# Kernel tuning notes

Measured on AMD Instinct MI355X. Metric: run time of the kernel, lower is better.

The kernel has to match this reference:

```python
import jax, jax.numpy as jnp
import numpy as np
from jax import lax

K, N = 256, 65536

def setup_inputs() -> dict:
    key = jax.random.key(0)
    k1, k2, k3 = jax.random.split(key, 3)
    # obs: non-negative event counts [K, N]
    obs = jax.random.uniform(k1, (K, N), dtype=jnp.float32) * 4.0
    # Beta ~ U(1, 3) [K]
    Beta = 1.0 + 2.0 * jax.random.uniform(k2, (K,), dtype=jnp.float32)
    # Alpha ~ U(0, 0.01) [K, K]
    Alpha = 0.01 * jax.random.uniform(k3, (K, K), dtype=jnp.float32)
    return {"obs": obs, "Beta": Beta, "Alpha": Alpha}

def reference(obs, Beta, Alpha):
    # obs: [K, N], Beta: [K], Alpha: [K, K]
    Kk, Nn = obs.shape
    Mu0 = obs.mean(axis=1) / 10.0 + 0.01            # [K] background rate
    decay = jnp.exp(-Beta)                          # [K]

    # Exponential kernel sum S[t] = sum_{tp<t} obs[:,tp] * Beta * exp(-(t-tp)*Beta)
    # admits recursion H[t] = exp(-Beta) * (H[t-1] + obs[:, t-1]), S[t] = Beta * H[t]
    def step(h, o_prev):
        h_new = decay * (h + o_prev)
        return h_new, h_new

    _, H = lax.scan(step, jnp.zeros((Kk,), obs.dtype), obs[:, :Nn - 1].T)  # [N-1, K]
    S = H * Beta                                    # [N-1, K]
    # lam1[:, t] = softplus(Alpha @ S[t]) for t >= 1; lam1[:, 0] = 0 (by original code)
    lam = jax.nn.softplus(jnp.einsum('jk,tk->tj', Alpha, S))  # [N-1, K]
    lams1 = jnp.concatenate([jnp.zeros((Kk, 1), obs.dtype), lam.T], axis=1)  # [K, N]
    lams0 = jnp.broadcast_to(Mu0[:, None], (Kk, Nn))          # [K, N]

    Nloglams = obs * jnp.log(lams0 + lams1 + 1e-5)
    loglik = (Nloglams - lams0 - lams1).sum()
    return loglik, lams0, lams1
```

## Files before the change

kernel.cpp:

```cpp
#include <hip/hip_runtime.h>
#include <math.h>

#define KK 256
#define NN 65536
#define TT 64
#define WW 48
#define TPAD 264

typedef __bf16 bf16x8 __attribute__((ext_vector_type(8)));
typedef float f32x4 __attribute__((ext_vector_type(4)));

__global__ __launch_bounds__(256) void rowsum_kernel(const float* __restrict__ obs,
                                                     float* __restrict__ partial) {
  const int b = blockIdx.x;
  const int r = b >> 3, e = b & 7;
  const int tid = threadIdx.x;
  const float4* p = (const float4*)(obs + (size_t)r * NN + e * 8192) + tid;
  float s = 0.f;
#pragma unroll
  for (int i = 0; i < 8; ++i) {
    float4 v = p[i * 256];
    s += (v.x + v.y) + (v.z + v.w);
  }
  __shared__ float red[256];
  red[tid] = s;
  __syncthreads();
  for (int off = 128; off > 0; off >>= 1) {
    if (tid < off) red[tid] += red[tid + off];
    __syncthreads();
  }
  if (tid == 0) partial[b] = red[0];
}

__global__ __launch_bounds__(256) void prep_kernel(const float* __restrict__ Alpha,
                                                   const float* __restrict__ partial,
                                                   float* __restrict__ mu0,
                                                   __bf16* __restrict__ AlphaB,
                                                   float* __restrict__ out) {
  const int j = blockIdx.x;
  const int tid = threadIdx.x;
  AlphaB[(size_t)j * KK + tid] = (__bf16)Alpha[(size_t)j * KK + tid];
  if (tid == 0) {
    float s = 0.f;
#pragma unroll
    for (int i = 0; i < 8; ++i) s += partial[j * 8 + i];
    mu0[j] = s * (1.0f / NN) * 0.1f + 0.01f;
    if (j == 0) out[0] = 0.f;
  }
}

__global__ __launch_bounds__(256, 2) void main_kernel(const float* __restrict__ obs,
                                                      const float* __restrict__ Beta,
                                                      const float* __restrict__ mu0,
                                                      const __bf16* __restrict__ AlphaB,
                                                      float* __restrict__ out) {
  __shared__ __bf16 Slds[TT][TPAD];
  const int tid = threadIdx.x;
  const int t0 = blockIdx.x * TT;

  {
    const int k = tid;
    const float beta = Beta[k];
    const float decay = expf(-beta);
    const float* row = obs + (size_t)k * NN;
    float g = 0.f;
    if (t0 > 0) {
      const float4* p = (const float4*)(row + t0 - WW);
#pragma unroll
      for (int i = 0; i < WW / 4; ++i) {
        float4 v = p[i];
        g = decay * (g + v.x);
        g = decay * (g + v.y);
        g = decay * (g + v.z);
        g = decay * (g + v.w);
      }
    }
    Slds[0][k] = (__bf16)(beta * g);
    const float4* q = (const float4*)(row + t0);
#pragma unroll
    for (int i = 0; i < 15; ++i) {
      float4 v = q[i];
      g = decay * (g + v.x); Slds[4 * i + 1][k] = (__bf16)(beta * g);
      g = decay * (g + v.y); Slds[4 * i + 2][k] = (__bf16)(beta * g);
      g = decay * (g + v.z); Slds[4 * i + 3][k] = (__bf16)(beta * g);
      g = decay * (g + v.w); Slds[4 * i + 4][k] = (__bf16)(beta * g);
    }
    {
      float4 v = q[15];
      g = decay * (g + v.x); Slds[61][k] = (__bf16)(beta * g);
      g = decay * (g + v.y); Slds[62][k] = (__bf16)(beta * g);
      g = decay * (g + v.z); Slds[63][k] = (__bf16)(beta * g);
    }
  }
  __syncthreads();

  const int wave = tid >> 6;
  const int lane = tid & 63;
  const int lquad = lane >> 4;
  const int l16 = lane & 15;

  f32x4 acc[4][4];
#pragma unroll
  for (int a = 0; a < 4; ++a)
#pragma unroll
    for (int b = 0; b < 4; ++b) acc[a][b] = (f32x4){0.f, 0.f, 0.f, 0.f};

  const __bf16* Abase = AlphaB + (size_t)(wave * 64 + l16) * KK + lquad * 8;
  for (int k0 = 0; k0 < KK; k0 += 32) {
    bf16x8 afrag[4], bfrag[4];
#pragma unroll
    for (int js = 0; js < 4; ++js)
      afrag[js] = *(const bf16x8*)(Abase + (size_t)js * 16 * KK + k0);
#pragma unroll
    for (int ts = 0; ts < 4; ++ts)
      bfrag[ts] = *(const bf16x8*)&Slds[ts * 16 + l16][k0 + lquad * 8];
#pragma unroll
    for (int js = 0; js < 4; ++js)
#pragma unroll
      for (int ts = 0; ts < 4; ++ts)
        acc[js][ts] = __builtin_amdgcn_mfma_f32_16x16x32_bf16(
            afrag[js], bfrag[ts], acc[js][ts], 0, 0, 0);
  }

  float partial = 0.f;
  float* lams0 = out + 1;
  float* lams1 = out + 1 + (size_t)KK * NN;
#pragma unroll
  for (int js = 0; js < 4; ++js) {
#pragma unroll
    for (int r = 0; r < 4; ++r) {
      const int j = wave * 64 + js * 16 + lquad * 4 + r;
      const float m = mu0[j];
      const size_t rowoff = (size_t)j * NN + t0 + l16;
#pragma unroll
      for (int ts = 0; ts < 4; ++ts) {
        float v = acc[js][ts][r];
        float lam = v + __logf(1.f + __expf(-v));
        if (t0 + ts * 16 + l16 == 0) lam = 0.f;
        lams1[rowoff + ts * 16] = lam;
        lams0[rowoff + ts * 16] = m;
        const float o = obs[rowoff + ts * 16];
        partial += o * __logf(m + lam + 1e-5f) - m - lam;
      }
    }
  }

#pragma unroll
  for (int off = 32; off > 0; off >>= 1)
    partial += __shfl_down(partial, off, 64);
  if (lane == 0) atomicAdd(out, partial);
}

extern "C" void kernel_launch(void* const* d_in, const int* in_sizes, int n_in,
                              void* d_out, int out_size, void* d_ws, size_t ws_size,
                              hipStream_t stream) {
  const float* obs   = (const float*)d_in[0];
  const float* Beta  = (const float*)d_in[1];
  const float* Alpha = (const float*)d_in[2];
  float* out = (float*)d_out;

  float* partial = (float*)d_ws;
  float* mu0 = partial + 2048;
  __bf16* AlphaB = (__bf16*)(mu0 + 256);

  hipLaunchKernelGGL(rowsum_kernel, dim3(KK * 8), dim3(256), 0, stream, obs, partial);
  hipLaunchKernelGGL(prep_kernel, dim3(KK), dim3(256), 0, stream, Alpha, partial,
                     mu0, AlphaB, out);
  hipLaunchKernelGGL(main_kernel, dim3(NN / TT), dim3(256), 0, stream,
                     obs, Beta, mu0, AlphaB, out);
}
```

Measured before the change: 276.8 us.

## Split scan into separate kernel writing S to global, fuse row sums into scan

Moves the exponential-decay recurrence out of the GEMM kernel into a dedicated scan kernel over 128-step tiles. It writes bf16 S[t][k] to a global workspace and computes per-tile row sums, which replaces the separate rowsum pass over obs. The GEMM kernel then reads B fragments straight from global S instead of LDS, with no shared memory and a higher occupancy hint. The intent is to cut the warm-up recompute and redundant obs reads. The cost is an extra global write and read of S (32 MB of bf16) plus a transposed partial-sum reduction in prep.

```diff
diff --git a/kernel.cpp b/kernel.cpp
--- a/kernel.cpp
+++ b/kernel.cpp
@@ -3,33 +3,60 @@
 
 #define KK 256
 #define NN 65536
-#define TT 64
 #define WW 48
-#define TPAD 264
+#define TA 128
+#define TG 64
+#define NTILE (NN / TA)
 
 typedef __bf16 bf16x8 __attribute__((ext_vector_type(8)));
 typedef float f32x4 __attribute__((ext_vector_type(4)));
 
-__global__ __launch_bounds__(256) void rowsum_kernel(const float* __restrict__ obs,
-                                                     float* __restrict__ partial) {
-  const int b = blockIdx.x;
-  const int r = b >> 3, e = b & 7;
-  const int tid = threadIdx.x;
-  const float4* p = (const float4*)(obs + (size_t)r * NN + e * 8192) + tid;
-  float s = 0.f;
+__global__ __launch_bounds__(256) void scan_kernel(const float* __restrict__ obs,
+                                                   const float* __restrict__ Beta,
+                                                   __bf16* __restrict__ ST,
+                                                   float* __restrict__ partial) {
+  const int c = blockIdx.x;
+  const int k = threadIdx.x;
+  const int t0 = c * TA;
+  const float beta = Beta[k];
+  const float decay = __expf(-beta);
+  const float* row = obs + (size_t)k * NN;
+
+  float g = 0.f;
+  if (t0 > 0) {
+    const float4* p = (const float4*)(row + t0 - WW);
 #pragma unroll
-  for (int i = 0; i < 8; ++i) {
-    float4 v = p[i * 256];
-    s += (v.x + v.y) + (v.z + v.w);
+    for (int i = 0; i < WW / 4; ++i) {
+      float4 v = p[i];
+      g = decay * (g + v.x);
+      g = decay * (g + v.y);
+      g = decay * (g + v.z);
+      g = decay * (g + v.w);
+    }
   }
-  __shared__ float red[256];
-  red[tid] = s;
-  __syncthreads();
-  for (int off = 128; off > 0; off >>= 1) {
-    if (tid < off) red[tid] += red[tid + off];
-    __syncthreads();
+
+  __bf16* st = ST + (size_t)t0 * KK + k;
+  st[0] = (__bf16)(beta * g);
+
+  float rsum = 0.f;
+  const float4* q = (const float4*)(row + t0);
+#pragma unroll 4
+  for (int i = 0; i < TA / 4 - 1; ++i) {
+    float4 v = q[i];
+    rsum += (v.x + v.y) + (v.z + v.w);
+    g = decay * (g + v.x); st[(size_t)(4 * i + 1) * KK] = (__bf16)(beta * g);
+    g = decay * (g + v.y); st[(size_t)(4 * i + 2) * KK] = (__bf16)(beta * g);
+    g = decay * (g + v.z); st[(size_t)(4 * i + 3) * KK] = (__bf16)(beta * g);
+    g = decay * (g + v.w); st[(size_t)(4 * i + 4) * KK] = (__bf16)(beta * g);
   }
-  if (tid == 0) partial[b] = red[0];
+  {
+    float4 v = q[TA / 4 - 1];
+    rsum += (v.x + v.y) + (v.z + v.w);
+    g = decay * (g + v.x); st[(size_t)(TA - 3) * KK] = (__bf16)(beta * g);
+    g = decay * (g + v.y); st[(size_t)(TA - 2) * KK] = (__bf16)(beta * g);
+    g = decay * (g + v.z); st[(size_t)(TA - 1) * KK] = (__bf16)(beta * g);
+  }
+  partial[c * KK + k] = rsum;
 }
 
 __global__ __launch_bounds__(256) void prep_kernel(const float* __restrict__ Alpha,
@@ -40,60 +67,27 @@
   const int j = blockIdx.x;
   const int tid = threadIdx.x;
   AlphaB[(size_t)j * KK + tid] = (__bf16)Alpha[(size_t)j * KK + tid];
+  float s = partial[(size_t)tid * KK + j] + partial[(size_t)(tid + 256) * KK + j];
+  __shared__ float red[256];
+  red[tid] = s;
+  __syncthreads();
+  for (int off = 128; off > 0; off >>= 1) {
+    if (tid < off) red[tid] += red[tid + off];
+    __syncthreads();
+  }
   if (tid == 0) {
-    float s = 0.f;
-#pragma unroll
-    for (int i = 0; i < 8; ++i) s += partial[j * 8 + i];
-    mu0[j] = s * (1.0f / NN) * 0.1f + 0.01f;
+    mu0[j] = red[0] * (1.0f / NN) * 0.1f + 0.01f;
     if (j == 0) out[0] = 0.f;
   }
 }
 
-__global__ __launch_bounds__(256, 2) void main_kernel(const float* __restrict__ obs,
-                                                      const float* __restrict__ Beta,
+__global__ __launch_bounds__(256, 4) void gemm_kernel(const float* __restrict__ obs,
                                                       const float* __restrict__ mu0,
                                                       const __bf16* __restrict__ AlphaB,
+                                                      const __bf16* __restrict__ ST,
                                                       float* __restrict__ out) {
-  __shared__ __bf16 Slds[TT][TPAD];
   const int tid = threadIdx.x;
-  const int t0 = blockIdx.x * TT;
-
-  {
-    const int k = tid;
-    const float beta = Beta[k];
-    const float decay = expf(-beta);
-    const float* row = obs + (size_t)k * NN;
-    float g = 0.f;
-    if (t0 > 0) {
-      const float4* p = (const float4*)(row + t0 - WW);
-#pragma unroll
-      for (int i = 0; i < WW / 4; ++i) {
-        float4 v = p[i];
-        g = decay * (g + v.x);
-        g = decay * (g + v.y);
-        g = decay * (g + v.z);
-        g = decay * (g + v.w);
-      }
-    }
-    Slds[0][k] = (__bf16)(beta * g);
-    const float4* q = (const float4*)(row + t0);
-#pragma unroll
-    for (int i = 0; i < 15; ++i) {
-      float4 v = q[i];
-      g = decay * (g + v.x); Slds[4 * i + 1][k] = (__bf16)(beta * g);
-      g = decay * (g + v.y); Slds[4 * i + 2][k] = (__bf16)(beta * g);
-      g = decay * (g + v.z); Slds[4 * i + 3][k] = (__bf16)(beta * g);
-      g = decay * (g + v.w); Slds[4 * i + 4][k] = (__bf16)(beta * g);
-    }
-    {
-      float4 v = q[15];
-      g = decay * (g + v.x); Slds[61][k] = (__bf16)(beta * g);
-      g = decay * (g + v.y); Slds[62][k] = (__bf16)(beta * g);
-      g = decay * (g + v.z); Slds[63][k] = (__bf16)(beta * g);
-    }
-  }
-  __syncthreads();
-
+  const int t0 = blockIdx.x * TG;
   const int wave = tid >> 6;
   const int lane = tid & 63;
   const int lquad = lane >> 4;
@@ -106,6 +100,8 @@
     for (int b = 0; b < 4; ++b) acc[a][b] = (f32x4){0.f, 0.f, 0.f, 0.f};
 
   const __bf16* Abase = AlphaB + (size_t)(wave * 64 + l16) * KK + lquad * 8;
+  const __bf16* Bbase = ST + (size_t)(t0 + l16) * KK + lquad * 8;
+#pragma unroll
   for (int k0 = 0; k0 < KK; k0 += 32) {
     bf16x8 afrag[4], bfrag[4];
 #pragma unroll
@@ -113,7 +109,7 @@
       afrag[js] = *(const bf16x8*)(Abase + (size_t)js * 16 * KK + k0);
 #pragma unroll
     for (int ts = 0; ts < 4; ++ts)
-      bfrag[ts] = *(const bf16x8*)&Slds[ts * 16 + l16][k0 + lquad * 8];
+      bfrag[ts] = *(const bf16x8*)(Bbase + (size_t)ts * 16 * KK + k0);
 #pragma unroll
     for (int js = 0; js < 4; ++js)
 #pragma unroll
@@ -160,12 +156,14 @@
   float* out = (float*)d_out;
 
   float* partial = (float*)d_ws;
-  float* mu0 = partial + 2048;
+  float* mu0 = partial + NTILE * KK;
   __bf16* AlphaB = (__bf16*)(mu0 + 256);
+  __bf16* ST = AlphaB + KK * KK;
 
-  hipLaunchKernelGGL(rowsum_kernel, dim3(KK * 8), dim3(256), 0, stream, obs, partial);
-  hipLaunchKernelGGL(prep_kernel, dim3(KK), dim3(256), 0, stream, Alpha, partial,
-                     mu0, AlphaB, out);
-  hipLaunchKernelGGL(main_kernel, dim3(NN / TT), dim3(256), 0, stream,
-                     obs, Beta, mu0, AlphaB, out);
+  hipLaunchKernelGGL(scan_kernel, dim3(NTILE), dim3(256), 0, stream,
+                     obs, Beta, ST, partial);
+  hipLaunchKernelGGL(prep_kernel, dim3(KK), dim3(256), 0, stream,
+                     Alpha, partial, mu0, AlphaB, out);
+  hipLaunchKernelGGL(gemm_kernel, dim3(NN / TG), dim3(256), 0, stream,
+                     obs, mu0, AlphaB, ST, out);
 }
```

Measured after the change: 316.1 us. 1.14x slower.
